# Kernel optimization log

Hardware: AMD Instinct MI355X
Metric: run time of the kernel (lower is better)

## Reference

```python
import jax, jax.numpy as jnp
import numpy as np

N_NODES = 200_000
N_EDGES = 6_400_000
N_GRAPHS = 1024
F_IN = 16
H1 = 8
H2 = 16
STEPS = 4


def setup_inputs() -> dict:
    key = jax.random.key(0)
    ks = jax.random.split(key, 16)
    x = jax.random.normal(ks[0], (N_NODES, F_IN), jnp.float32)
    edge_index = jax.random.randint(ks[1], (2, N_EDGES), 0, N_NODES, dtype=jnp.int64)
    batch = jnp.sort(jax.random.randint(ks[2], (N_NODES,), 0, N_GRAPHS, dtype=jnp.int64))

    def p(k, shape):
        return jax.random.normal(k, shape, jnp.float32) * 0.1

    return {
        "x": x, "edge_index": edge_index, "batch": batch,
        # SAGEConv1: lin_l (neighbors, with bias) + lin_r (root, no bias)
        "W1l": p(ks[3], (H1, F_IN)), "b1l": jnp.zeros((H1,), jnp.float32), "W1r": p(ks[4], (H1, F_IN)),
        # SAGEConv2
        "W2l": p(ks[5], (H2, H1)), "b2l": jnp.zeros((H2,), jnp.float32), "W2r": p(ks[6], (H2, H1)),
        # Set2Set LSTM: input 2*H2, hidden H2, torch gate order (i, f, g, o)
        "Wih": p(ks[7], (4 * H2, 2 * H2)), "Whh": p(ks[8], (4 * H2, H2)),
        "bih": jnp.zeros((4 * H2,), jnp.float32), "bhh": jnp.zeros((4 * H2,), jnp.float32),
        # Final fc: 2*H2 -> 2
        "Wfc": p(ks[9], (2, 2 * H2)), "bfc": jnp.zeros((2,), jnp.float32),
    }


def _sage_conv(x, src, dst, Wl, bl, Wr):
    # PyG SAGEConv (mean aggr): out = lin_l(mean_j x_j) + lin_r(x_i)
    n = x.shape[0]
    agg = jax.ops.segment_sum(x[src], dst, num_segments=n)          # [N, F]
    deg = jax.ops.segment_sum(jnp.ones_like(dst, dtype=x.dtype), dst, num_segments=n)
    agg = agg / jnp.maximum(deg, 1.0)[:, None]
    return agg @ Wl.T + bl + x @ Wr.T


def _set2set(x, batch, Wih, Whh, bih, bhh):
    # order-invariant pooling with iterative content attention
    B = N_GRAPHS
    h = jnp.zeros((B, H2), x.dtype)
    c = jnp.zeros((B, H2), x.dtype)
    q_star = jnp.zeros((B, 2 * H2), x.dtype)
    for _ in range(STEPS):
        gates = q_star @ Wih.T + bih + h @ Whh.T + bhh
        i, f, g, o = jnp.split(gates, 4, axis=-1)
        c = jax.nn.sigmoid(f) * c + jax.nn.sigmoid(i) * jnp.tanh(g)
        h = jax.nn.sigmoid(o) * jnp.tanh(c)
        q = h                                                      # [B, H2]
        e = jnp.sum(x * q[batch], axis=-1)                         # [N]
        emax = jax.ops.segment_max(e, batch, num_segments=B)
        a = jnp.exp(e - emax[batch])
        asum = jax.ops.segment_sum(a, batch, num_segments=B)
        a = a / asum[batch]                                        # segment softmax
        r = jax.ops.segment_sum(a[:, None] * x, batch, num_segments=B)  # [B, H2]
        q_star = jnp.concatenate([q, r], axis=-1)
    return q_star


def reference(x, edge_index, batch, W1l, b1l, W1r, W2l, b2l, W2r,
              Wih, Whh, bih, bhh, Wfc, bfc):
    src, dst = edge_index[0], edge_index[1]
    x = jax.nn.relu(_sage_conv(x, src, dst, W1l, b1l, W1r))
    x = jax.nn.relu(_sage_conv(x, src, dst, W2l, b2l, W2r))
    q_star = _set2set(x, batch, Wih, Whh, bih, bhh)
    return q_star @ Wfc.T + bfc
```

## Files before the change

kernel.cpp:

```cpp
#include <hip/hip_runtime.h>

#define N_NODES 200000
#define N_EDGES 6400000
#define N_GRAPHS 1024
#define F_IN 16
#define H1 8
#define H2 16
#define STEPS 4

#define NB 1024
#define BNODES 196
#define NSLAB 8
#define CAPS 1024
#define BSLOTS (NSLAB * CAPS)
#define CAP 7680
#define SMAX 320
#define RPT 16
#define RPADD 200

typedef _Float16 half8 __attribute__((ext_vector_type(8)));

__global__ void k_y1(const float* __restrict__ x, const float* __restrict__ W1l,
                     _Float16* __restrict__ y1) {
    int n = blockIdx.x * blockDim.x + threadIdx.x;
    if (n >= N_NODES) return;
    float xv[F_IN];
#pragma unroll
    for (int k = 0; k < F_IN; k++) xv[k] = x[(long long)n * F_IN + k];
    half8 o;
#pragma unroll
    for (int j = 0; j < H1; j++) {
        float s = 0.f;
#pragma unroll
        for (int k = 0; k < F_IN; k++) s += W1l[j * F_IN + k] * xv[k];
        o[j] = (_Float16)s;
    }
    *(half8*)&y1[(long long)n * H1] = o;
}

#define FILL_T 16384
__global__ __launch_bounds__(1024) void k_bin_fill(const int* __restrict__ src,
                                                   const int* __restrict__ dst,
                                                   int* __restrict__ gcur8,
                                                   unsigned int* __restrict__ grec) {
    __shared__ int scnt[NB];
    __shared__ int soff[NB];
    int tid = threadIdx.x;
    int slab = blockIdx.x & (NSLAB - 1);
    long long ebase = (long long)blockIdx.x * FILL_T;
    scnt[tid] = 0;
    __syncthreads();
    unsigned int rec[16];
    unsigned int meta[16];
#pragma unroll
    for (int u = 0; u < 16; u++) {
        long long e = ebase + (long long)u * 1024 + tid;
        if (e < N_EDGES) {
            int d = __builtin_nontemporal_load(dst + e);
            int s = __builtin_nontemporal_load(src + e);
            int b = d / BNODES;
            int dl = d - b * BNODES;
            rec[u] = ((unsigned int)s << 8) | (unsigned int)dl;
            int r = atomicAdd(&scnt[b], 1);
            meta[u] = ((unsigned int)b << 16) | (unsigned int)r;
        } else {
            meta[u] = 0xFFFFFFFFu;
        }
    }
    __syncthreads();
    {
        int c = scnt[tid];
        soff[tid] = c ? atomicAdd(&gcur8[tid * NSLAB + slab], c) : 0;
    }
    __syncthreads();
#pragma unroll
    for (int u = 0; u < 16; u++) {
        if (meta[u] != 0xFFFFFFFFu) {
            int b = meta[u] >> 16;
            unsigned int slot = (unsigned int)soff[b] + (meta[u] & 0xFFFFu);
            if (slot < CAPS)
                grec[(size_t)b * BSLOTS + slab * CAPS + slot] = rec[u];
        }
    }
}

__device__ __forceinline__ void block_scan_hist(const int* hist, int* start,
                                                int tid, int* wsum) {
    int v = (tid < BNODES) ? hist[tid] : 0;
    int lane = tid & 63, w = tid >> 6;
    int s = v;
#pragma unroll
    for (int off = 1; off < 64; off <<= 1) {
        int u = __shfl_up(s, off);
        if (lane >= off) s += u;
    }
    if (lane == 63) wsum[w] = s;
    __syncthreads();
    int base = 0;
    for (int i = 0; i < w; i++) base += wsum[i];
    s += base;
    if (tid < BNODES) start[tid] = s - v;
    if (tid == 511) start[BNODES] = s;
    __syncthreads();
}

__global__ __launch_bounds__(512) void k_conv1(
    const float* __restrict__ x, const _Float16* __restrict__ y1,
    const int* __restrict__ gcur8, unsigned int* __restrict__ grec,
    int* __restrict__ growptr,
    const float* __restrict__ b1l, const float* __restrict__ W1r,
    _Float16* __restrict__ h1) {
    __shared__ int lsrc[CAP];
    __shared__ int hist[BNODES];
    __shared__ int start[BNODES + 1];
    __shared__ int wsum[8];
    __shared__ int cnt8[NSLAB];
    int b = blockIdx.x, tid = threadIdx.x;
    size_t base = (size_t)b * BSLOTS;
    if (tid < NSLAB) {
        int c = gcur8[b * NSLAB + tid];
        cnt8[tid] = c > CAPS ? CAPS : c;
    }
    for (int j = tid; j < BNODES; j += 512) hist[j] = 0;
    __syncthreads();
    unsigned int rec[RPT];
#pragma unroll
    for (int u = 0; u < RPT; u++) {
        int idx = u * 512 + tid;
        int s = idx >> 10, slot = idx & (CAPS - 1);
        if (slot < cnt8[s]) {
            rec[u] = __builtin_nontemporal_load(grec + base + idx);
            atomicAdd(&hist[rec[u] & 255], 1);
        } else {
            rec[u] = 0xFFFFFFFFu;
        }
    }
    __syncthreads();
    block_scan_hist(hist, start, tid, wsum);
    for (int j = tid; j < BNODES; j += 512) hist[j] = 0;
    __syncthreads();
#pragma unroll
    for (int u = 0; u < RPT; u++) {
        if (rec[u] != 0xFFFFFFFFu) {
            int dl = rec[u] & 255;
            int k = atomicAdd(&hist[dl], 1);
            lsrc[start[dl] + k] = (int)(rec[u] >> 8);
        }
    }
    __syncthreads();
    int total = start[BNODES];
    for (int j = tid; j < total; j += 512)
        __builtin_nontemporal_store((unsigned int)lsrc[j], grec + base + j);
    if (tid <= BNODES) growptr[b * RPADD + tid] = start[tid];
    if (tid < 2 * BNODES) {
        int dl = tid >> 1, half = tid & 1;
        int n = b * BNODES + dl;
        int s0 = start[dl], s1 = start[dl + 1];
        int mid = s0 + ((s1 - s0) >> 1);
        int ga = half ? mid : s0;
        int gb = half ? s1 : mid;
        float acc[H1];
#pragma unroll
        for (int k = 0; k < H1; k++) acc[k] = 0.f;
        int e = ga;
        for (; e + 4 <= gb; e += 4) {
            int a0 = lsrc[e], a1 = lsrc[e + 1], a2 = lsrc[e + 2], a3 = lsrc[e + 3];
            half8 v0 = *(const half8*)&y1[(long long)a0 * H1];
            half8 v1 = *(const half8*)&y1[(long long)a1 * H1];
            half8 v2 = *(const half8*)&y1[(long long)a2 * H1];
            half8 v3 = *(const half8*)&y1[(long long)a3 * H1];
#pragma unroll
            for (int k = 0; k < H1; k++)
                acc[k] += ((float)v0[k] + (float)v1[k]) + ((float)v2[k] + (float)v3[k]);
        }
        for (; e < gb; e++) {
            half8 v = *(const half8*)&y1[(long long)lsrc[e] * H1];
#pragma unroll
            for (int k = 0; k < H1; k++) acc[k] += (float)v[k];
        }
#pragma unroll
        for (int k = 0; k < H1; k++) acc[k] += __shfl_xor(acc[k], 1);
        if (half == 0 && n < N_NODES) {
            float inv = 1.0f / fmaxf((float)(s1 - s0), 1.0f);
            float xv[F_IN];
#pragma unroll
            for (int k = 0; k < F_IN; k++) xv[k] = x[(long long)n * F_IN + k];
            half8 o;
#pragma unroll
            for (int j = 0; j < H1; j++) {
                float s = acc[j] * inv + b1l[j];
#pragma unroll
                for (int k = 0; k < F_IN; k++) s += W1r[j * F_IN + k] * xv[k];
                o[j] = (_Float16)fmaxf(s, 0.0f);
            }
            *(half8*)&h1[(long long)n * H1] = o;
        }
    }
}

__global__ __launch_bounds__(512) void k_conv2(
    const _Float16* __restrict__ h1,
    const unsigned int* __restrict__ gsorted, const int* __restrict__ growptr,
    const float* __restrict__ b2l, const float* __restrict__ W2l,
    const float* __restrict__ W2r, float* __restrict__ h2) {
    int b = blockIdx.x, tid = threadIdx.x;
    if (tid >= 2 * BNODES) return;
    int dl = tid >> 1, half = tid & 1;
    int n = b * BNODES + dl;
    if (n >= N_NODES) return;
    int s0 = __builtin_nontemporal_load(growptr + b * RPADD + dl);
    int s1 = __builtin_nontemporal_load(growptr + b * RPADD + dl + 1);
    const unsigned int* seg = gsorted + (size_t)b * BSLOTS;
    int mid = s0 + ((s1 - s0) >> 1);
    int ga = half ? mid : s0;
    int gb = half ? s1 : mid;
    float acc[H1];
#pragma unroll
    for (int k = 0; k < H1; k++) acc[k] = 0.f;
    int e = ga;
    for (; e + 4 <= gb; e += 4) {
        int a0 = __builtin_nontemporal_load(seg + e);
        int a1 = __builtin_nontemporal_load(seg + e + 1);
        int a2 = __builtin_nontemporal_load(seg + e + 2);
        int a3 = __builtin_nontemporal_load(seg + e + 3);
        half8 v0 = *(const half8*)&h1[(long long)a0 * H1];
        half8 v1 = *(const half8*)&h1[(long long)a1 * H1];
        half8 v2 = *(const half8*)&h1[(long long)a2 * H1];
        half8 v3 = *(const half8*)&h1[(long long)a3 * H1];
#pragma unroll
        for (int k = 0; k < H1; k++)
            acc[k] += ((float)v0[k] + (float)v1[k]) + ((float)v2[k] + (float)v3[k]);
    }
    for (; e < gb; e++) {
        int a = __builtin_nontemporal_load(seg + e);
        half8 v = *(const half8*)&h1[(long long)a * H1];
#pragma unroll
        for (int k = 0; k < H1; k++) acc[k] += (float)v[k];
    }
#pragma unroll
    for (int k = 0; k < H1; k++) acc[k] += __shfl_xor(acc[k], 1);
    if (half == 0) {
        float inv = 1.0f / fmaxf((float)(s1 - s0), 1.0f);
        float av[H1], hv[H1];
        half8 hr = *(const half8*)&h1[(long long)n * H1];
#pragma unroll
        for (int k = 0; k < H1; k++) { hv[k] = (float)hr[k]; av[k] = acc[k] * inv; }
        float o[H2];
#pragma unroll
        for (int j = 0; j < H2; j++) {
            float s = b2l[j];
#pragma unroll
            for (int k = 0; k < H1; k++) s += W2l[j * H1 + k] * av[k] + W2r[j * H1 + k] * hv[k];
            o[j] = fmaxf(s, 0.0f);
        }
        *(float4*)&h2[(long long)n * H2] = make_float4(o[0], o[1], o[2], o[3]);
        *(float4*)&h2[(long long)n * H2 + 4] = make_float4(o[4], o[5], o[6], o[7]);
        *(float4*)&h2[(long long)n * H2 + 8] = make_float4(o[8], o[9], o[10], o[11]);
        *(float4*)&h2[(long long)n * H2 + 12] = make_float4(o[12], o[13], o[14], o[15]);
    }
}

__global__ void k_ptr(const int* __restrict__ batch, int* __restrict__ ptr) {
    int n = blockIdx.x * blockDim.x + threadIdx.x;
    if (n >= N_NODES) return;
    int b = batch[n];
    int bp = (n == 0) ? -1 : batch[n - 1];
    for (int g = bp + 1; g <= b; g++) ptr[g] = n;
    if (n == N_NODES - 1) {
        for (int g = b + 1; g <= N_GRAPHS; g++) ptr[g] = N_NODES;
    }
}

__global__ __launch_bounds__(256) void k_set2set(
    const float* __restrict__ h2, const int* __restrict__ ptr,
    const float* __restrict__ Wih, const float* __restrict__ Whh,
    const float* __restrict__ bih, const float* __restrict__ bhh,
    const float* __restrict__ Wfc, const float* __restrict__ bfc,
    float* __restrict__ out) {
    int b = blockIdx.x;
    int start = ptr[b], end = ptr[b + 1], cnt = end - start;
    __shared__ float sx[SMAX][H2 + 1];
    __shared__ float el[SMAX];
    __shared__ float sh[H2], sc[H2], sq[2 * H2], sg[4 * H2];
    __shared__ float red[4][17];
    __shared__ float s_emax, s_asum, s_r[H2];
    int tid = threadIdx.x;
    int wid = tid >> 6, lane = tid & 63;
    bool fit = (cnt <= SMAX);

    if (fit) {
        for (int i = start + tid; i < end; i += 256) {
            const float4* p = (const float4*)&h2[(long long)i * H2];
            float4 r0 = p[0], r1 = p[1], r2 = p[2], r3 = p[3];
            float* row = sx[i - start];
            row[0] = r0.x; row[1] = r0.y; row[2] = r0.z; row[3] = r0.w;
            row[4] = r1.x; row[5] = r1.y; row[6] = r1.z; row[7] = r1.w;
            row[8] = r2.x; row[9] = r2.y; row[10] = r2.z; row[11] = r2.w;
            row[12] = r3.x; row[13] = r3.y; row[14] = r3.z; row[15] = r3.w;
        }
    }
    if (tid < H2) { sh[tid] = 0.f; sc[tid] = 0.f; }
    if (tid < 2 * H2) sq[tid] = 0.f;
    __syncthreads();

    for (int step = 0; step < STEPS; step++) {
        if (tid < 64) {
            float g = bih[tid] + bhh[tid];
#pragma unroll
            for (int k = 0; k < 2 * H2; k++) g += Wih[tid * (2 * H2) + k] * sq[k];
#pragma unroll
            for (int k = 0; k < H2; k++) g += Whh[tid * H2 + k] * sh[k];
            sg[tid] = g;
        }
        __syncthreads();
        if (tid < H2) {
            float ig = 1.f / (1.f + expf(-sg[tid]));
            float fg = 1.f / (1.f + expf(-sg[H2 + tid]));
            float gg = tanhf(sg[2 * H2 + tid]);
            float og = 1.f / (1.f + expf(-sg[3 * H2 + tid]));
            float cc = fg * sc[tid] + ig * gg;
            sc[tid] = cc;
            sh[tid] = og * tanhf(cc);
        }
        __syncthreads();

        float lmax = -3.0e38f;
        if (fit) {
            for (int ii = tid; ii < cnt; ii += 256) {
                float e = 0.f;
#pragma unroll
                for (int k = 0; k < H2; k++) e += sx[ii][k] * sh[k];
                el[ii] = e;
                lmax = fmaxf(lmax, e);
            }
        } else {
            for (int i = start + tid; i < end; i += 256) {
                float e = 0.f;
#pragma unroll
                for (int k = 0; k < H2; k++) e += h2[(long long)i * H2 + k] * sh[k];
                lmax = fmaxf(lmax, e);
            }
        }
        for (int off = 32; off; off >>= 1) lmax = fmaxf(lmax, __shfl_down(lmax, off));
        if (lane == 0) red[wid][0] = lmax;
        __syncthreads();
        if (tid == 0) {
            float m = red[0][0];
            for (int w = 1; w < 4; w++) m = fmaxf(m, red[w][0]);
            s_emax = m;
        }
        __syncthreads();
        float emax = s_emax;

        float asum = 0.f, rloc[H2];
#pragma unroll
        for (int k = 0; k < H2; k++) rloc[k] = 0.f;
        if (fit) {
            for (int ii = tid; ii < cnt; ii += 256) {
                float a = expf(el[ii] - emax);
                asum += a;
#pragma unroll
                for (int k = 0; k < H2; k++) rloc[k] += a * sx[ii][k];
            }
        } else {
            for (int i = start + tid; i < end; i += 256) {
                float hv[H2];
                float e = 0.f;
#pragma unroll
                for (int k = 0; k < H2; k++) { hv[k] = h2[(long long)i * H2 + k]; e += hv[k] * sh[k]; }
                float a = expf(e - emax);
                asum += a;
#pragma unroll
                for (int k = 0; k < H2; k++) rloc[k] += a * hv[k];
            }
        }
        for (int off = 32; off; off >>= 1) {
            asum += __shfl_down(asum, off);
#pragma unroll
            for (int k = 0; k < H2; k++) rloc[k] += __shfl_down(rloc[k], off);
        }
        if (lane == 0) {
            red[wid][16] = asum;
#pragma unroll
            for (int k = 0; k < H2; k++) red[wid][k] = rloc[k];
        }
        __syncthreads();
        if (tid < 17) {
            float s = red[0][tid] + red[1][tid] + red[2][tid] + red[3][tid];
            if (tid == 16) s_asum = s; else s_r[tid] = s;
        }
        __syncthreads();
        if (tid < H2) {
            float rr = (cnt > 0 && s_asum > 0.f) ? s_r[tid] / s_asum : 0.0f;
            sq[tid] = sh[tid];
            sq[H2 + tid] = rr;
        }
        __syncthreads();
    }

    if (tid < 2) {
        float s = bfc[tid];
#pragma unroll
        for (int k = 0; k < 2 * H2; k++) s += Wfc[tid * (2 * H2) + k] * sq[k];
        out[b * 2 + tid] = s;
    }
}

extern "C" void kernel_launch(void* const* d_in, const int* in_sizes, int n_in,
                              void* d_out, int out_size, void* d_ws, size_t ws_size,
                              hipStream_t stream) {
    const float* x   = (const float*)d_in[0];
    const int*   ei  = (const int*)d_in[1];
    const int*   src = ei;
    const int*   dst = ei + N_EDGES;
    const int*   batch = (const int*)d_in[2];
    const float* W1l = (const float*)d_in[3];
    const float* b1l = (const float*)d_in[4];
    const float* W1r = (const float*)d_in[5];
    const float* W2l = (const float*)d_in[6];
    const float* b2l = (const float*)d_in[7];
    const float* W2r = (const float*)d_in[8];
    const float* Wih = (const float*)d_in[9];
    const float* Whh = (const float*)d_in[10];
    const float* bih = (const float*)d_in[11];
    const float* bhh = (const float*)d_in[12];
    const float* Wfc = (const float*)d_in[13];
    const float* bfc = (const float*)d_in[14];
    float* out = (float*)d_out;

    char* ws = (char*)d_ws;
    unsigned int* grec = (unsigned int*)ws;
    int* gcur8 = (int*)(grec + (size_t)NB * BSLOTS);
    int* growptr = gcur8 + NB * NSLAB;
    _Float16* y1 = (_Float16*)(growptr + (size_t)NB * RPADD);
    _Float16* h1 = y1 + (size_t)N_NODES * H1;
    float* h2  = (float*)(h1 + (size_t)N_NODES * H1);
    int*   ptr = (int*)(h2 + (size_t)N_NODES * H2);

    hipMemsetAsync(gcur8, 0, (size_t)NB * NSLAB * sizeof(int), stream);

    int nb_node = (N_NODES + 255) / 256;
    int nb_fill = (int)(((long long)N_EDGES + FILL_T - 1) / FILL_T);

    k_y1<<<nb_node, 256, 0, stream>>>(x, W1l, y1);
    k_bin_fill<<<nb_fill, 1024, 0, stream>>>(src, dst, gcur8, grec);
    k_conv1<<<NB, 512, 0, stream>>>(x, y1, gcur8, grec, growptr, b1l, W1r, h1);
    k_conv2<<<NB, 512, 0, stream>>>(h1, grec, growptr, b2l, W2l, W2r, h2);
    k_ptr<<<nb_node, 256, 0, stream>>>(batch, ptr);
    k_set2set<<<N_GRAPHS, 256, 0, stream>>>(h2, ptr, Wih, Whh, bih, bhh, Wfc, bfc, out);
}
```

Baseline: 205.7 us.

## Pad per-node edge lists to multiples of four with zero-row sentinel for vector loads

Each destination node's neighbour list in the CSR segments is padded to a multiple of four entries, filled with an index pointing to an added all-zero feature row. This lets conv1 and conv2 read neighbour indices as 16-byte vectors and drop the scalar tail loop. Offset and length are packed into one growptr word, so conv2 does fewer loads. In exchange it adds padding gathers, more LDS use, and a fill pass over the shared list.

New measurement: 201.0 us. 1.02x faster.

```diff
diff --git a/kernel.cpp b/kernel.cpp
--- a/kernel.cpp
+++ b/kernel.cpp
@@ -13,17 +13,25 @@
 #define NSLAB 8
 #define CAPS 1024
 #define BSLOTS (NSLAB * CAPS)
-#define CAP 7680
+#define CAP 8784
 #define SMAX 320
 #define RPT 16
 #define RPADD 200
+#define ZIDX N_NODES
 
 typedef _Float16 half8 __attribute__((ext_vector_type(8)));
+typedef int int4v __attribute__((ext_vector_type(4)));
 
 __global__ void k_y1(const float* __restrict__ x, const float* __restrict__ W1l,
-                     _Float16* __restrict__ y1) {
+                     _Float16* __restrict__ y1, _Float16* __restrict__ h1) {
     int n = blockIdx.x * blockDim.x + threadIdx.x;
-    if (n >= N_NODES) return;
+    if (n > N_NODES) return;
+    if (n == N_NODES) {
+        half8 z = {};
+        *(half8*)&y1[(long long)ZIDX * H1] = z;
+        *(half8*)&h1[(long long)ZIDX * H1] = z;
+        return;
+    }
     float xv[F_IN];
 #pragma unroll
     for (int k = 0; k < F_IN; k++) xv[k] = x[(long long)n * F_IN + k];
@@ -84,35 +92,16 @@
     }
 }
 
-__device__ __forceinline__ void block_scan_hist(const int* hist, int* start,
-                                                int tid, int* wsum) {
-    int v = (tid < BNODES) ? hist[tid] : 0;
-    int lane = tid & 63, w = tid >> 6;
-    int s = v;
-#pragma unroll
-    for (int off = 1; off < 64; off <<= 1) {
-        int u = __shfl_up(s, off);
-        if (lane >= off) s += u;
-    }
-    if (lane == 63) wsum[w] = s;
-    __syncthreads();
-    int base = 0;
-    for (int i = 0; i < w; i++) base += wsum[i];
-    s += base;
-    if (tid < BNODES) start[tid] = s - v;
-    if (tid == 511) start[BNODES] = s;
-    __syncthreads();
-}
-
 __global__ __launch_bounds__(512) void k_conv1(
     const float* __restrict__ x, const _Float16* __restrict__ y1,
     const int* __restrict__ gcur8, unsigned int* __restrict__ grec,
     int* __restrict__ growptr,
     const float* __restrict__ b1l, const float* __restrict__ W1r,
     _Float16* __restrict__ h1) {
-    __shared__ int lsrc[CAP];
+    __shared__ __align__(16) int lsrc[CAP];
     __shared__ int hist[BNODES];
     __shared__ int start[BNODES + 1];
+    __shared__ int slen[BNODES];
     __shared__ int wsum[8];
     __shared__ int cnt8[NSLAB];
     int b = blockIdx.x, tid = threadIdx.x;
@@ -136,8 +125,35 @@
         }
     }
     __syncthreads();
-    block_scan_hist(hist, start, tid, wsum);
+    {
+        int v = (tid < BNODES) ? hist[tid] : 0;
+        int pl = (v + 3) & ~3;
+        int lane = tid & 63, w = tid >> 6;
+        int s = pl;
+#pragma unroll
+        for (int off = 1; off < 64; off <<= 1) {
+            int u = __shfl_up(s, off);
+            if (lane >= off) s += u;
+        }
+        if (lane == 63) wsum[w] = s;
+        __syncthreads();
+        int bb = 0;
+        for (int i = 0; i < w; i++) bb += wsum[i];
+        s += bb;
+        int ps = s - pl;
+        if (tid < BNODES) {
+            start[tid] = ps; slen[tid] = v;
+            growptr[b * RPADD + tid] = (ps << 16) | v;
+        }
+        if (tid == BNODES) {
+            start[tid] = ps;
+            growptr[b * RPADD + tid] = (ps << 16);
+        }
+    }
+    __syncthreads();
+    int ptotal = start[BNODES];
     for (int j = tid; j < BNODES; j += 512) hist[j] = 0;
+    for (int j = tid; j < ptotal; j += 512) lsrc[j] = ZIDX;
     __syncthreads();
 #pragma unroll
     for (int u = 0; u < RPT; u++) {
@@ -148,40 +164,37 @@
         }
     }
     __syncthreads();
-    int total = start[BNODES];
-    for (int j = tid; j < total; j += 512)
-        __builtin_nontemporal_store((unsigned int)lsrc[j], grec + base + j);
-    if (tid <= BNODES) growptr[b * RPADD + tid] = start[tid];
+    {
+        int pe = ptotal > BSLOTS ? BSLOTS : ptotal;
+        for (int j = tid * 4; j < pe; j += 2048) {
+            int4v vv = *(const int4v*)&lsrc[j];
+            __builtin_nontemporal_store(vv, (int4v*)(grec + base + j));
+        }
+    }
     if (tid < 2 * BNODES) {
         int dl = tid >> 1, half = tid & 1;
         int n = b * BNODES + dl;
-        int s0 = start[dl], s1 = start[dl + 1];
-        int mid = s0 + ((s1 - s0) >> 1);
-        int ga = half ? mid : s0;
-        int gb = half ? s1 : mid;
+        int ps0 = start[dl];
+        int nblk = (start[dl + 1] - ps0) >> 2;
+        int c0 = half ? (nblk >> 1) : 0;
+        int c1 = half ? nblk : (nblk >> 1);
         float acc[H1];
 #pragma unroll
         for (int k = 0; k < H1; k++) acc[k] = 0.f;
-        int e = ga;
-        for (; e + 4 <= gb; e += 4) {
-            int a0 = lsrc[e], a1 = lsrc[e + 1], a2 = lsrc[e + 2], a3 = lsrc[e + 3];
-            half8 v0 = *(const half8*)&y1[(long long)a0 * H1];
-            half8 v1 = *(const half8*)&y1[(long long)a1 * H1];
-            half8 v2 = *(const half8*)&y1[(long long)a2 * H1];
-            half8 v3 = *(const half8*)&y1[(long long)a3 * H1];
+        for (int blk = c0; blk < c1; blk++) {
+            int4v a = *(const int4v*)&lsrc[ps0 + 4 * blk];
+            half8 v0 = *(const half8*)&y1[(long long)a.x * H1];
+            half8 v1 = *(const half8*)&y1[(long long)a.y * H1];
+            half8 v2 = *(const half8*)&y1[(long long)a.z * H1];
+            half8 v3 = *(const half8*)&y1[(long long)a.w * H1];
 #pragma unroll
             for (int k = 0; k < H1; k++)
                 acc[k] += ((float)v0[k] + (float)v1[k]) + ((float)v2[k] + (float)v3[k]);
         }
-        for (; e < gb; e++) {
-            half8 v = *(const half8*)&y1[(long long)lsrc[e] * H1];
-#pragma unroll
-            for (int k = 0; k < H1; k++) acc[k] += (float)v[k];
-        }
 #pragma unroll
         for (int k = 0; k < H1; k++) acc[k] += __shfl_xor(acc[k], 1);
         if (half == 0 && n < N_NODES) {
-            float inv = 1.0f / fmaxf((float)(s1 - s0), 1.0f);
+            float inv = 1.0f / fmaxf((float)slen[dl], 1.0f);
             float xv[F_IN];
 #pragma unroll
             for (int k = 0; k < F_IN; k++) xv[k] = x[(long long)n * F_IN + k];
@@ -208,39 +221,30 @@
     int dl = tid >> 1, half = tid & 1;
     int n = b * BNODES + dl;
     if (n >= N_NODES) return;
-    int s0 = __builtin_nontemporal_load(growptr + b * RPADD + dl);
-    int s1 = __builtin_nontemporal_load(growptr + b * RPADD + dl + 1);
-    const unsigned int* seg = gsorted + (size_t)b * BSLOTS;
-    int mid = s0 + ((s1 - s0) >> 1);
-    int ga = half ? mid : s0;
-    int gb = half ? s1 : mid;
+    int pack0 = growptr[b * RPADD + dl];
+    int pack1 = growptr[b * RPADD + dl + 1];
+    int ps0 = pack0 >> 16, sl = pack0 & 0xFFFF;
+    int nblk = ((pack1 >> 16) - ps0) >> 2;
+    const int4v* seg4 = (const int4v*)(gsorted + (size_t)b * BSLOTS + ps0);
+    int c0 = half ? (nblk >> 1) : 0;
+    int c1 = half ? nblk : (nblk >> 1);
     float acc[H1];
 #pragma unroll
     for (int k = 0; k < H1; k++) acc[k] = 0.f;
-    int e = ga;
-    for (; e + 4 <= gb; e += 4) {
-        int a0 = __builtin_nontemporal_load(seg + e);
-        int a1 = __builtin_nontemporal_load(seg + e + 1);
-        int a2 = __builtin_nontemporal_load(seg + e + 2);
-        int a3 = __builtin_nontemporal_load(seg + e + 3);
-        half8 v0 = *(const half8*)&h1[(long long)a0 * H1];
-        half8 v1 = *(const half8*)&h1[(long long)a1 * H1];
-        half8 v2 = *(const half8*)&h1[(long long)a2 * H1];
-        half8 v3 = *(const half8*)&h1[(long long)a3 * H1];
+    for (int blk = c0; blk < c1; blk++) {
+        int4v a = __builtin_nontemporal_load(seg4 + blk);
+        half8 v0 = *(const half8*)&h1[(long long)a.x * H1];
+        half8 v1 = *(const half8*)&h1[(long long)a.y * H1];
+        half8 v2 = *(const half8*)&h1[(long long)a.z * H1];
+        half8 v3 = *(const half8*)&h1[(long long)a.w * H1];
 #pragma unroll
         for (int k = 0; k < H1; k++)
             acc[k] += ((float)v0[k] + (float)v1[k]) + ((float)v2[k] + (float)v3[k]);
     }
-    for (; e < gb; e++) {
-        int a = __builtin_nontemporal_load(seg + e);
-        half8 v = *(const half8*)&h1[(long long)a * H1];
-#pragma unroll
-        for (int k = 0; k < H1; k++) acc[k] += (float)v[k];
-    }
 #pragma unroll
     for (int k = 0; k < H1; k++) acc[k] += __shfl_xor(acc[k], 1);
     if (half == 0) {
-        float inv = 1.0f / fmaxf((float)(s1 - s0), 1.0f);
+        float inv = 1.0f / fmaxf((float)sl, 1.0f);
         float av[H1], hv[H1];
         half8 hr = *(const half8*)&h1[(long long)n * H1];
 #pragma unroll
@@ -433,16 +437,17 @@
     int* gcur8 = (int*)(grec + (size_t)NB * BSLOTS);
     int* growptr = gcur8 + NB * NSLAB;
     _Float16* y1 = (_Float16*)(growptr + (size_t)NB * RPADD);
-    _Float16* h1 = y1 + (size_t)N_NODES * H1;
-    float* h2  = (float*)(h1 + (size_t)N_NODES * H1);
+    _Float16* h1 = y1 + (size_t)(N_NODES + 4) * H1;
+    float* h2  = (float*)(h1 + (size_t)(N_NODES + 4) * H1);
     int*   ptr = (int*)(h2 + (size_t)N_NODES * H2);
 
     hipMemsetAsync(gcur8, 0, (size_t)NB * NSLAB * sizeof(int), stream);
 
+    int nb_node1 = (N_NODES + 1 + 255) / 256;
     int nb_node = (N_NODES + 255) / 256;
     int nb_fill = (int)(((long long)N_EDGES + FILL_T - 1) / FILL_T);
 
-    k_y1<<<nb_node, 256, 0, stream>>>(x, W1l, y1);
+    k_y1<<<nb_node1, 256, 0, stream>>>(x, W1l, y1, h1);
     k_bin_fill<<<nb_fill, 1024, 0, stream>>>(src, dst, gcur8, grec);
     k_conv1<<<NB, 512, 0, stream>>>(x, y1, gcur8, grec, growptr, b1l, W1r, h1);
     k_conv2<<<NB, 512, 0, stream>>>(h1, grec, growptr, b2l, W2l, W2r, h2);
```
